# Kernel tuning notes

Measured on AMD Instinct MI355X. Metric: run time of the kernel, lower is better.

## Reference

```python
import jax, jax.numpy as jnp
import numpy as np

MASK_VALUE = -1e6


def setup_inputs() -> dict:
    key = jax.random.key(0)
    ks = jax.random.split(key, 8)
    B, Lq, Lk, D, H = 4, 512, 512, 128, 128
    return {
        "queries": jax.random.normal(ks[0], (B, Lq, D), dtype=jnp.float32),
        "keys": jax.random.normal(ks[1], (B, Lk, D), dtype=jnp.float32),
        "values": jax.random.normal(ks[2], (B, Lk, D), dtype=jnp.float32),
        "valid_seq_len": jax.random.randint(ks[3], (B,), 1, Lk + 1),
        "Wq": jax.random.normal(ks[4], (D, H), dtype=jnp.float32) * 0.05,
        "Wk": jax.random.normal(ks[5], (D, H), dtype=jnp.float32) * 0.05,
        "wv": jax.random.normal(ks[6], (H,), dtype=jnp.float32) * 0.05,
        "Wo": jax.random.normal(ks[7], (D, H), dtype=jnp.float32) * 0.05,
    }


def reference(queries, keys, values, valid_seq_len, Wq, Wk, wv, Wo):
    # q: (B,Lq,H), k: (B,Lk,H)
    q = jnp.einsum("bqd,dh->bqh", queries, Wq)
    k = jnp.einsum("bkd,dh->bkh", keys, Wk)
    # additive features: (B,Lq,Lk,H) -> scalar scores via wv
    feat = jnp.tanh(q[:, :, None, :] + k[:, None, :, :])
    scores = jnp.einsum("bqkh,h->bqk", feat, wv)
    # mask invalid key positions per batch (softmax over last dim)
    Lk = keys.shape[1]
    mask = jnp.arange(Lk)[None, None, :] < valid_seq_len[:, None, None]
    scores = jnp.where(mask, scores, MASK_VALUE)
    attn = jax.nn.softmax(scores, axis=-1)  # (B,Lq,Lk)
    out = jnp.einsum("bqk,bkd->bqd", attn, values)
    return jnp.einsum("bqd,dh->bqh", out, Wo)
```

## Files before the change

### kernel.cpp

```cpp
#include <hip/hip_runtime.h>
#include <hip/hip_bf16.h>

#define B_  4
#define LQ  512
#define LK  512
#define D_  128
#define H_  128
#define TQ  4

#define TWO_LOG2E 2.885390081777927f
#define LOG2E     1.442695040888963f

__device__ __forceinline__ float fexp2(float x) {
#if __has_builtin(__builtin_amdgcn_exp2f)
  return __builtin_amdgcn_exp2f(x);
#else
  return exp2f(x);
#endif
}
__device__ __forceinline__ float frcp(float x) {
#if __has_builtin(__builtin_amdgcn_rcpf)
  return __builtin_amdgcn_rcpf(x);
#else
  return __fdividef(1.0f, x);
#endif
}

__global__ __launch_bounds__(256) void proj_kernel(
    const float* __restrict__ queries, const float* __restrict__ keys,
    const float* __restrict__ Wq, const float* __restrict__ Wk,
    float* __restrict__ qproj, float* __restrict__ kT) {
  __shared__ float s_x[8][D_];
  int r0 = blockIdx.x * 8;
  bool qside = r0 < B_ * LQ;
  const float* X = qside ? queries : keys;
  const float* W = qside ? Wq : Wk;
  int rb = qside ? r0 : r0 - B_ * LQ;
  int tid = threadIdx.x;
  for (int i = tid; i < 8 * D_; i += 256)
    s_x[i >> 7][i & 127] = X[(size_t)(rb + (i >> 7)) * D_ + (i & 127)];
  __syncthreads();
  int h = tid & 127, rh = tid >> 7;
  float a0 = 0.f, a1 = 0.f, a2 = 0.f, a3 = 0.f;
  #pragma unroll 8
  for (int d = 0; d < D_; ++d) {
    float w = W[d * H_ + h];
    a0 += s_x[rh * 4 + 0][d] * w;
    a1 += s_x[rh * 4 + 1][d] * w;
    a2 += s_x[rh * 4 + 2][d] * w;
    a3 += s_x[rh * 4 + 3][d] * w;
  }
  if (qside) {
    qproj[(size_t)(rb + rh * 4 + 0) * H_ + h] = a0 * TWO_LOG2E;
    qproj[(size_t)(rb + rh * 4 + 1) * H_ + h] = a1 * TWO_LOG2E;
    qproj[(size_t)(rb + rh * 4 + 2) * H_ + h] = a2 * TWO_LOG2E;
    qproj[(size_t)(rb + rh * 4 + 3) * H_ + h] = a3 * TWO_LOG2E;
  } else {
    int b = rb >> 9, kk = (rb & 511) + rh * 4;
    float* dst = kT + ((size_t)b * H_ + h) * LK + kk;
    dst[0] = a0 * TWO_LOG2E;
    dst[1] = a1 * TWO_LOG2E;
    dst[2] = a2 * TWO_LOG2E;
    dst[3] = a3 * TWO_LOG2E;
  }
}

__global__ __launch_bounds__(512, 4) void attn_kernel(
    const float* __restrict__ qproj, const float* __restrict__ kT,
    const float* __restrict__ values, const int* __restrict__ vlen_arr,
    const float* __restrict__ wv, const float* __restrict__ Wo,
    float* __restrict__ out) {
  int b  = blockIdx.y;
  int q0 = blockIdx.x * TQ;
  int tid = threadIdx.x;

  __shared__ float s_q[TQ][H_];
  __shared__ float s_wv[H_];
  __shared__ float s_sc[TQ][LK];
  __shared__ float s_po[2][TQ][D_];

  for (int i = tid; i < TQ * H_; i += 512)
    s_q[i >> 7][i & 127] = qproj[(size_t)(b * LQ + q0 + (i >> 7)) * H_ + (i & 127)];
  if (tid < H_) s_wv[tid] = wv[tid];
  __syncthreads();
  int vlen = vlen_arr[b];

  const float4* wv4p = (const float4*)s_wv;
  float sum_wv = 0.f;
  #pragma unroll
  for (int j = 0; j < H_ / 4; ++j) {
    float4 t = wv4p[j];
    sum_wv += t.x + t.y + t.z + t.w;
  }

  {
    int kt = tid & 255, qs = tid >> 8;
    int k  = kt * 2;
    if (k < vlen) {
      const float2* kTp = (const float2*)(kT + (size_t)b * H_ * LK);
      const float4* qap = (const float4*)s_q[qs * 2 + 0];
      const float4* qbp = (const float4*)s_q[qs * 2 + 1];
      float a00 = 0.f, a10 = 0.f, a01 = 0.f, a11 = 0.f;
      #pragma unroll 4
      for (int h4 = 0; h4 < H_ / 4; ++h4) {
        float2 kv0 = kTp[(size_t)(4 * h4 + 0) * 256 + kt];
        float2 kv1 = kTp[(size_t)(4 * h4 + 1) * 256 + kt];
        float2 kv2 = kTp[(size_t)(4 * h4 + 2) * 256 + kt];
        float2 kv3 = kTp[(size_t)(4 * h4 + 3) * 256 + kt];
        float4 w4 = wv4p[h4];
        float4 qa = qap[h4];
        float4 qb = qbp[h4];
        a00 = fmaf(w4.x, frcp(fexp2(qa.x + kv0.x) + 1.f), a00);
        a10 = fmaf(w4.x, frcp(fexp2(qa.x + kv0.y) + 1.f), a10);
        a01 = fmaf(w4.x, frcp(fexp2(qb.x + kv0.x) + 1.f), a01);
        a11 = fmaf(w4.x, frcp(fexp2(qb.x + kv0.y) + 1.f), a11);
        a00 = fmaf(w4.y, frcp(fexp2(qa.y + kv1.x) + 1.f), a00);
        a10 = fmaf(w4.y, frcp(fexp2(qa.y + kv1.y) + 1.f), a10);
        a01 = fmaf(w4.y, frcp(fexp2(qb.y + kv1.x) + 1.f), a01);
        a11 = fmaf(w4.y, frcp(fexp2(qb.y + kv1.y) + 1.f), a11);
        a00 = fmaf(w4.z, frcp(fexp2(qa.z + kv2.x) + 1.f), a00);
        a10 = fmaf(w4.z, frcp(fexp2(qa.z + kv2.y) + 1.f), a10);
        a01 = fmaf(w4.z, frcp(fexp2(qb.z + kv2.x) + 1.f), a01);
        a11 = fmaf(w4.z, frcp(fexp2(qb.z + kv2.y) + 1.f), a11);
        a00 = fmaf(w4.w, frcp(fexp2(qa.w + kv3.x) + 1.f), a00);
        a10 = fmaf(w4.w, frcp(fexp2(qa.w + kv3.y) + 1.f), a10);
        a01 = fmaf(w4.w, frcp(fexp2(qb.w + kv3.x) + 1.f), a01);
        a11 = fmaf(w4.w, frcp(fexp2(qb.w + kv3.y) + 1.f), a11);
      }
      bool m1 = (k + 1) < vlen;
      float2 r0 = { fmaf(-2.f, a00, sum_wv), m1 ? fmaf(-2.f, a10, sum_wv) : -1.0e6f };
      float2 r1 = { fmaf(-2.f, a01, sum_wv), m1 ? fmaf(-2.f, a11, sum_wv) : -1.0e6f };
      ((float2*)s_sc[qs * 2 + 0])[kt] = r0;
      ((float2*)s_sc[qs * 2 + 1])[kt] = r1;
    } else {
      float2 mm = { -1.0e6f, -1.0e6f };
      ((float2*)s_sc[qs * 2 + 0])[kt] = mm;
      ((float2*)s_sc[qs * 2 + 1])[kt] = mm;
    }
  }
  __syncthreads();

  int wave = tid >> 6, lane = tid & 63;

  if (wave < TQ) {
    float m = -3.0e38f;
    #pragma unroll
    for (int j = 0; j < LK / 64; ++j) m = fmaxf(m, s_sc[wave][lane + j * 64]);
    #pragma unroll
    for (int off = 32; off; off >>= 1) m = fmaxf(m, __shfl_xor(m, off));
    float sum = 0.f;
    float vals[LK / 64];
    #pragma unroll
    for (int j = 0; j < LK / 64; ++j) {
      float e = fexp2((s_sc[wave][lane + j * 64] - m) * LOG2E);
      vals[j] = e;
      sum += e;
    }
    #pragma unroll
    for (int off = 32; off; off >>= 1) sum += __shfl_xor(sum, off);
    float inv = frcp(sum);
    #pragma unroll
    for (int j = 0; j < LK / 64; ++j) s_sc[wave][lane + j * 64] = vals[j] * inv;
  }
  __syncthreads();

  {
    int row = wave >> 1, kc = wave & 1;
    int kend = min((((vlen + 3) >> 2) << 2), (kc + 1) * 256);
    const float2* vrow = (const float2*)(values + (size_t)b * LK * D_);
    float2 a = {0.f, 0.f};
    for (int k = kc * 256; k < kend; k += 4) {
      float4 sc4 = *((const float4*)&s_sc[row][k]);
      float2 v0 = vrow[(size_t)(k + 0) * 64 + lane];
      float2 v1 = vrow[(size_t)(k + 1) * 64 + lane];
      float2 v2 = vrow[(size_t)(k + 2) * 64 + lane];
      float2 v3 = vrow[(size_t)(k + 3) * 64 + lane];
      a.x += sc4.x * v0.x + sc4.y * v1.x + sc4.z * v2.x + sc4.w * v3.x;
      a.y += sc4.x * v0.y + sc4.y * v1.y + sc4.z * v2.y + sc4.w * v3.y;
    }
    s_po[kc][row][2 * lane]     = a.x;
    s_po[kc][row][2 * lane + 1] = a.y;
  }
  __syncthreads();

  {
    int ql = tid >> 7, h = tid & 127;
    float acc = 0.f;
    #pragma unroll 8
    for (int d = 0; d < D_; ++d)
      acc += (s_po[0][ql][d] + s_po[1][ql][d]) * Wo[d * H_ + h];
    out[((size_t)b * LQ + q0 + ql) * H_ + h] = acc;
  }
}

extern "C" void kernel_launch(void* const* d_in, const int* in_sizes, int n_in,
                              void* d_out, int out_size, void* d_ws, size_t ws_size,
                              hipStream_t stream) {
  const float* queries = (const float*)d_in[0];
  const float* keys    = (const float*)d_in[1];
  const float* values  = (const float*)d_in[2];
  const int*   vlen    = (const int*)d_in[3];
  const float* Wq      = (const float*)d_in[4];
  const float* Wk      = (const float*)d_in[5];
  const float* wv      = (const float*)d_in[6];
  const float* Wo      = (const float*)d_in[7];
  float* out = (float*)d_out;

  float* qproj = (float*)d_ws;
  float* kT    = qproj + (size_t)B_ * LQ * H_;

  proj_kernel<<<dim3(B_ * (LQ + LK) / 8), 256, 0, stream>>>(queries, keys, Wq, Wk, qproj, kT);
  attn_kernel<<<dim3(LQ / TQ, B_), 512, 0, stream>>>(qproj, kT, values, vlen, wv, Wo, out);
}
```

Measured before the change: 130.9 us.

## Stage key projection tiles in double-buffered LDS and compute 4 queries per thread

The score phase now streams the transposed key projection through a double-buffered shared-memory tile of 16 hidden dims by all keys. The next tile's global load overlaps with the tanh/score computation on the current tile. Each thread now owns one key and all four queries, where before it handled two keys and two queries. The occupancy hint in launch_bounds is dropped, and shared memory grows by 64 KB per block, which may limit how many blocks fit per CU. A barrier per tile is added, and the global load stays unconditional even when a block's valid length is short.

```diff
diff --git a/kernel.cpp b/kernel.cpp
--- a/kernel.cpp
+++ b/kernel.cpp
@@ -7,6 +7,8 @@
 #define D_  128
 #define H_  128
 #define TQ  4
+#define HT  16
+#define NT  (H_ / HT)
 
 #define TWO_LOG2E 2.885390081777927f
 #define LOG2E     1.442695040888963f
@@ -65,7 +67,7 @@
   }
 }
 
-__global__ __launch_bounds__(512, 4) void attn_kernel(
+__global__ __launch_bounds__(512) void attn_kernel(
     const float* __restrict__ qproj, const float* __restrict__ kT,
     const float* __restrict__ values, const int* __restrict__ vlen_arr,
     const float* __restrict__ wv, const float* __restrict__ Wo,
@@ -74,6 +76,7 @@
   int q0 = blockIdx.x * TQ;
   int tid = threadIdx.x;
 
+  __shared__ float s_kt[2][HT][LK];
   __shared__ float s_q[TQ][H_];
   __shared__ float s_wv[H_];
   __shared__ float s_sc[TQ][LK];
@@ -82,6 +85,16 @@
   for (int i = tid; i < TQ * H_; i += 512)
     s_q[i >> 7][i & 127] = qproj[(size_t)(b * LQ + q0 + (i >> 7)) * H_ + (i & 127)];
   if (tid < H_) s_wv[tid] = wv[tid];
+
+  const float4* kt4 = (const float4*)(kT + (size_t)b * H_ * LK);
+
+  {
+    float4 r[4];
+    #pragma unroll
+    for (int j = 0; j < 4; ++j) r[j] = kt4[j * 512 + tid];
+    #pragma unroll
+    for (int j = 0; j < 4; ++j) ((float4*)s_kt[0])[j * 512 + tid] = r[j];
+  }
   __syncthreads();
   int vlen = vlen_arr[b];
 
@@ -89,54 +102,64 @@
   float sum_wv = 0.f;
   #pragma unroll
   for (int j = 0; j < H_ / 4; ++j) {
-    float4 t = wv4p[j];
-    sum_wv += t.x + t.y + t.z + t.w;
-  }
-
-  {
-    int kt = tid & 255, qs = tid >> 8;
-    int k  = kt * 2;
+    float4 t4 = wv4p[j];
+    sum_wv += t4.x + t4.y + t4.z + t4.w;
+  }
+
+  int k = tid;
+  float acc[TQ] = {0.f, 0.f, 0.f, 0.f};
+  for (int t = 0; t < NT; ++t) {
+    int cur = t & 1;
+    float4 r[4];
+    if (t + 1 < NT) {
+      const float4* src = kt4 + (size_t)(t + 1) * (HT * LK / 4);
+      #pragma unroll
+      for (int j = 0; j < 4; ++j) r[j] = src[j * 512 + tid];
+    }
     if (k < vlen) {
-      const float2* kTp = (const float2*)(kT + (size_t)b * H_ * LK);
-      const float4* qap = (const float4*)s_q[qs * 2 + 0];
-      const float4* qbp = (const float4*)s_q[qs * 2 + 1];
-      float a00 = 0.f, a10 = 0.f, a01 = 0.f, a11 = 0.f;
-      #pragma unroll 4
-      for (int h4 = 0; h4 < H_ / 4; ++h4) {
-        float2 kv0 = kTp[(size_t)(4 * h4 + 0) * 256 + kt];
-        float2 kv1 = kTp[(size_t)(4 * h4 + 1) * 256 + kt];
-        float2 kv2 = kTp[(size_t)(4 * h4 + 2) * 256 + kt];
-        float2 kv3 = kTp[(size_t)(4 * h4 + 3) * 256 + kt];
-        float4 w4 = wv4p[h4];
-        float4 qa = qap[h4];
-        float4 qb = qbp[h4];
-        a00 = fmaf(w4.x, frcp(fexp2(qa.x + kv0.x) + 1.f), a00);
-        a10 = fmaf(w4.x, frcp(fexp2(qa.x + kv0.y) + 1.f), a10);
-        a01 = fmaf(w4.x, frcp(fexp2(qb.x + kv0.x) + 1.f), a01);
-        a11 = fmaf(w4.x, frcp(fexp2(qb.x + kv0.y) + 1.f), a11);
-        a00 = fmaf(w4.y, frcp(fexp2(qa.y + kv1.x) + 1.f), a00);
-        a10 = fmaf(w4.y, frcp(fexp2(qa.y + kv1.y) + 1.f), a10);
-        a01 = fmaf(w4.y, frcp(fexp2(qb.y + kv1.x) + 1.f), a01);
-        a11 = fmaf(w4.y, frcp(fexp2(qb.y + kv1.y) + 1.f), a11);
-        a00 = fmaf(w4.z, frcp(fexp2(qa.z + kv2.x) + 1.f), a00);
-        a10 = fmaf(w4.z, frcp(fexp2(qa.z + kv2.y) + 1.f), a10);
-        a01 = fmaf(w4.z, frcp(fexp2(qb.z + kv2.x) + 1.f), a01);
-        a11 = fmaf(w4.z, frcp(fexp2(qb.z + kv2.y) + 1.f), a11);
-        a00 = fmaf(w4.w, frcp(fexp2(qa.w + kv3.x) + 1.f), a00);
-        a10 = fmaf(w4.w, frcp(fexp2(qa.w + kv3.y) + 1.f), a10);
-        a01 = fmaf(w4.w, frcp(fexp2(qb.w + kv3.x) + 1.f), a01);
-        a11 = fmaf(w4.w, frcp(fexp2(qb.w + kv3.y) + 1.f), a11);
+      #pragma unroll
+      for (int hh4 = 0; hh4 < HT / 4; ++hh4) {
+        int hb = t * HT + hh4 * 4;
+        float4 w4  = *(const float4*)&s_wv[hb];
+        float4 qv0 = *(const float4*)&s_q[0][hb];
+        float4 qv1 = *(const float4*)&s_q[1][hb];
+        float4 qv2 = *(const float4*)&s_q[2][hb];
+        float4 qv3 = *(const float4*)&s_q[3][hb];
+        float kv0 = s_kt[cur][hh4 * 4 + 0][k];
+        float kv1 = s_kt[cur][hh4 * 4 + 1][k];
+        float kv2 = s_kt[cur][hh4 * 4 + 2][k];
+        float kv3 = s_kt[cur][hh4 * 4 + 3][k];
+        acc[0] = fmaf(w4.x, frcp(fexp2(qv0.x + kv0) + 1.f), acc[0]);
+        acc[1] = fmaf(w4.x, frcp(fexp2(qv1.x + kv0) + 1.f), acc[1]);
+        acc[2] = fmaf(w4.x, frcp(fexp2(qv2.x + kv0) + 1.f), acc[2]);
+        acc[3] = fmaf(w4.x, frcp(fexp2(qv3.x + kv0) + 1.f), acc[3]);
+        acc[0] = fmaf(w4.y, frcp(fexp2(qv0.y + kv1) + 1.f), acc[0]);
+        acc[1] = fmaf(w4.y, frcp(fexp2(qv1.y + kv1) + 1.f), acc[1]);
+        acc[2] = fmaf(w4.y, frcp(fexp2(qv2.y + kv1) + 1.f), acc[2]);
+        acc[3] = fmaf(w4.y, frcp(fexp2(qv3.y + kv1) + 1.f), acc[3]);
+        acc[0] = fmaf(w4.z, frcp(fexp2(qv0.z + kv2) + 1.f), acc[0]);
+        acc[1] = fmaf(w4.z, frcp(fexp2(qv1.z + kv2) + 1.f), acc[1]);
+        acc[2] = fmaf(w4.z, frcp(fexp2(qv2.z + kv2) + 1.f), acc[2]);
+        acc[3] = fmaf(w4.z, frcp(fexp2(qv3.z + kv2) + 1.f), acc[3]);
+        acc[0] = fmaf(w4.w, frcp(fexp2(qv0.w + kv3) + 1.f), acc[0]);
+        acc[1] = fmaf(w4.w, frcp(fexp2(qv1.w + kv3) + 1.f), acc[1]);
+        acc[2] = fmaf(w4.w, frcp(fexp2(qv2.w + kv3) + 1.f), acc[2]);
+        acc[3] = fmaf(w4.w, frcp(fexp2(qv3.w + kv3) + 1.f), acc[3]);
       }
-      bool m1 = (k + 1) < vlen;
-      float2 r0 = { fmaf(-2.f, a00, sum_wv), m1 ? fmaf(-2.f, a10, sum_wv) : -1.0e6f };
-      float2 r1 = { fmaf(-2.f, a01, sum_wv), m1 ? fmaf(-2.f, a11, sum_wv) : -1.0e6f };
-      ((float2*)s_sc[qs * 2 + 0])[kt] = r0;
-      ((float2*)s_sc[qs * 2 + 1])[kt] = r1;
-    } else {
-      float2 mm = { -1.0e6f, -1.0e6f };
-      ((float2*)s_sc[qs * 2 + 0])[kt] = mm;
-      ((float2*)s_sc[qs * 2 + 1])[kt] = mm;
-    }
+    }
+    if (t + 1 < NT) {
+      float4* dst = (float4*)s_kt[cur ^ 1];
+      #pragma unroll
+      for (int j = 0; j < 4; ++j) dst[j * 512 + tid] = r[j];
+    }
+    __syncthreads();
+  }
+  if (k < vlen) {
+    #pragma unroll
+    for (int q = 0; q < TQ; ++q) s_sc[q][k] = fmaf(-2.f, acc[q], sum_wv);
+  } else {
+    #pragma unroll
+    for (int q = 0; q < TQ; ++q) s_sc[q][k] = -1.0e6f;
   }
   __syncthreads();
 
@@ -169,12 +192,12 @@
     int kend = min((((vlen + 3) >> 2) << 2), (kc + 1) * 256);
     const float2* vrow = (const float2*)(values + (size_t)b * LK * D_);
     float2 a = {0.f, 0.f};
-    for (int k = kc * 256; k < kend; k += 4) {
-      float4 sc4 = *((const float4*)&s_sc[row][k]);
-      float2 v0 = vrow[(size_t)(k + 0) * 64 + lane];
-      float2 v1 = vrow[(size_t)(k + 1) * 64 + lane];
-      float2 v2 = vrow[(size_t)(k + 2) * 64 + lane];
-      float2 v3 = vrow[(size_t)(k + 3) * 64 + lane];
+    for (int kk = kc * 256; kk < kend; kk += 4) {
+      float4 sc4 = *((const float4*)&s_sc[row][kk]);
+      float2 v0 = vrow[(size_t)(kk + 0) * 64 + lane];
+      float2 v1 = vrow[(size_t)(kk + 1) * 64 + lane];
+      float2 v2 = vrow[(size_t)(kk + 2) * 64 + lane];
+      float2 v3 = vrow[(size_t)(kk + 3) * 64 + lane];
       a.x += sc4.x * v0.x + sc4.y * v1.x + sc4.z * v2.x + sc4.w * v3.x;
       a.y += sc4.x * v0.y + sc4.y * v1.y + sc4.z * v2.y + sc4.w * v3.y;
     }
@@ -185,11 +208,11 @@
 
   {
     int ql = tid >> 7, h = tid & 127;
-    float acc = 0.f;
+    float acc2 = 0.f;
     #pragma unroll 8
     for (int d = 0; d < D_; ++d)
-      acc += (s_po[0][ql][d] + s_po[1][ql][d]) * Wo[d * H_ + h];
-    out[((size_t)b * LQ + q0 + ql) * H_ + h] = acc;
+      acc2 += (s_po[0][ql][d] + s_po[1][ql][d]) * Wo[d * H_ + h];
+    out[((size_t)b * LQ + q0 + ql) * H_ + h] = acc2;
   }
 }
 
```

After: 135.4 us. 3.4% more time.

## Halve query tile per block and remap threads to one key each

Applied to the files above, without the earlier changes.

The query tile per attention block drops from 4 rows to 2, which doubles the grid. The score phase now gives each thread one key for both queries instead of two keys. The PV product is split into four key chunks reduced in shared memory, and the minimum-blocks launch bound is removed. The aim is more blocks and waves in flight to hide the exp/rcp and global-load latency, at the cost of half the reuse of kT and value loads, so global/L2 traffic roughly doubles.

```diff
diff --git a/kernel.cpp b/kernel.cpp
--- a/kernel.cpp
+++ b/kernel.cpp
@@ -6,7 +6,7 @@
 #define LK  512
 #define D_  128
 #define H_  128
-#define TQ  4
+#define TQ  2
 
 #define TWO_LOG2E 2.885390081777927f
 #define LOG2E     1.442695040888963f
@@ -65,7 +65,7 @@
   }
 }
 
-__global__ __launch_bounds__(512, 4) void attn_kernel(
+__global__ __launch_bounds__(512) void attn_kernel(
     const float* __restrict__ qproj, const float* __restrict__ kT,
     const float* __restrict__ values, const int* __restrict__ vlen_arr,
     const float* __restrict__ wv, const float* __restrict__ Wo,
@@ -77,11 +77,12 @@
   __shared__ float s_q[TQ][H_];
   __shared__ float s_wv[H_];
   __shared__ float s_sc[TQ][LK];
-  __shared__ float s_po[2][TQ][D_];
-
-  for (int i = tid; i < TQ * H_; i += 512)
-    s_q[i >> 7][i & 127] = qproj[(size_t)(b * LQ + q0 + (i >> 7)) * H_ + (i & 127)];
-  if (tid < H_) s_wv[tid] = wv[tid];
+  __shared__ float s_po[4][TQ][D_];
+
+  if (tid < TQ * H_)
+    s_q[tid >> 7][tid & 127] = qproj[(size_t)(b * LQ + q0 + (tid >> 7)) * H_ + (tid & 127)];
+  else if (tid < TQ * H_ + H_)
+    s_wv[tid - TQ * H_] = wv[tid - TQ * H_];
   __syncthreads();
   int vlen = vlen_arr[b];
 
@@ -89,54 +90,39 @@
   float sum_wv = 0.f;
   #pragma unroll
   for (int j = 0; j < H_ / 4; ++j) {
-    float4 t = wv4p[j];
-    sum_wv += t.x + t.y + t.z + t.w;
-  }
-
-  {
-    int kt = tid & 255, qs = tid >> 8;
-    int k  = kt * 2;
-    if (k < vlen) {
-      const float2* kTp = (const float2*)(kT + (size_t)b * H_ * LK);
-      const float4* qap = (const float4*)s_q[qs * 2 + 0];
-      const float4* qbp = (const float4*)s_q[qs * 2 + 1];
-      float a00 = 0.f, a10 = 0.f, a01 = 0.f, a11 = 0.f;
-      #pragma unroll 4
-      for (int h4 = 0; h4 < H_ / 4; ++h4) {
-        float2 kv0 = kTp[(size_t)(4 * h4 + 0) * 256 + kt];
-        float2 kv1 = kTp[(size_t)(4 * h4 + 1) * 256 + kt];
-        float2 kv2 = kTp[(size_t)(4 * h4 + 2) * 256 + kt];
-        float2 kv3 = kTp[(size_t)(4 * h4 + 3) * 256 + kt];
-        float4 w4 = wv4p[h4];
-        float4 qa = qap[h4];
-        float4 qb = qbp[h4];
-        a00 = fmaf(w4.x, frcp(fexp2(qa.x + kv0.x) + 1.f), a00);
-        a10 = fmaf(w4.x, frcp(fexp2(qa.x + kv0.y) + 1.f), a10);
-        a01 = fmaf(w4.x, frcp(fexp2(qb.x + kv0.x) + 1.f), a01);
-        a11 = fmaf(w4.x, frcp(fexp2(qb.x + kv0.y) + 1.f), a11);
-        a00 = fmaf(w4.y, frcp(fexp2(qa.y + kv1.x) + 1.f), a00);
-        a10 = fmaf(w4.y, frcp(fexp2(qa.y + kv1.y) + 1.f), a10);
-        a01 = fmaf(w4.y, frcp(fexp2(qb.y + kv1.x) + 1.f), a01);
-        a11 = fmaf(w4.y, frcp(fexp2(qb.y + kv1.y) + 1.f), a11);
-        a00 = fmaf(w4.z, frcp(fexp2(qa.z + kv2.x) + 1.f), a00);
-        a10 = fmaf(w4.z, frcp(fexp2(qa.z + kv2.y) + 1.f), a10);
-        a01 = fmaf(w4.z, frcp(fexp2(qb.z + kv2.x) + 1.f), a01);
-        a11 = fmaf(w4.z, frcp(fexp2(qb.z + kv2.y) + 1.f), a11);
-        a00 = fmaf(w4.w, frcp(fexp2(qa.w + kv3.x) + 1.f), a00);
-        a10 = fmaf(w4.w, frcp(fexp2(qa.w + kv3.y) + 1.f), a10);
-        a01 = fmaf(w4.w, frcp(fexp2(qb.w + kv3.x) + 1.f), a01);
-        a11 = fmaf(w4.w, frcp(fexp2(qb.w + kv3.y) + 1.f), a11);
-      }
-      bool m1 = (k + 1) < vlen;
-      float2 r0 = { fmaf(-2.f, a00, sum_wv), m1 ? fmaf(-2.f, a10, sum_wv) : -1.0e6f };
-      float2 r1 = { fmaf(-2.f, a01, sum_wv), m1 ? fmaf(-2.f, a11, sum_wv) : -1.0e6f };
-      ((float2*)s_sc[qs * 2 + 0])[kt] = r0;
-      ((float2*)s_sc[qs * 2 + 1])[kt] = r1;
-    } else {
-      float2 mm = { -1.0e6f, -1.0e6f };
-      ((float2*)s_sc[qs * 2 + 0])[kt] = mm;
-      ((float2*)s_sc[qs * 2 + 1])[kt] = mm;
-    }
+    float4 t4 = wv4p[j];
+    sum_wv += t4.x + t4.y + t4.z + t4.w;
+  }
+
+  int k = tid;
+  if (k < vlen) {
+    const float* kcol = kT + ((size_t)b * H_) * LK + k;
+    const float4* qap = (const float4*)s_q[0];
+    const float4* qbp = (const float4*)s_q[1];
+    float acc0 = 0.f, acc1 = 0.f;
+    #pragma unroll 4
+    for (int h4 = 0; h4 < H_ / 4; ++h4) {
+      float kv0 = kcol[(size_t)(4 * h4 + 0) * LK];
+      float kv1 = kcol[(size_t)(4 * h4 + 1) * LK];
+      float kv2 = kcol[(size_t)(4 * h4 + 2) * LK];
+      float kv3 = kcol[(size_t)(4 * h4 + 3) * LK];
+      float4 w4 = wv4p[h4];
+      float4 qa = qap[h4];
+      float4 qb = qbp[h4];
+      acc0 = fmaf(w4.x, frcp(fexp2(qa.x + kv0) + 1.f), acc0);
+      acc1 = fmaf(w4.x, frcp(fexp2(qb.x + kv0) + 1.f), acc1);
+      acc0 = fmaf(w4.y, frcp(fexp2(qa.y + kv1) + 1.f), acc0);
+      acc1 = fmaf(w4.y, frcp(fexp2(qb.y + kv1) + 1.f), acc1);
+      acc0 = fmaf(w4.z, frcp(fexp2(qa.z + kv2) + 1.f), acc0);
+      acc1 = fmaf(w4.z, frcp(fexp2(qb.z + kv2) + 1.f), acc1);
+      acc0 = fmaf(w4.w, frcp(fexp2(qa.w + kv3) + 1.f), acc0);
+      acc1 = fmaf(w4.w, frcp(fexp2(qb.w + kv3) + 1.f), acc1);
+    }
+    s_sc[0][k] = fmaf(-2.f, acc0, sum_wv);
+    s_sc[1][k] = fmaf(-2.f, acc1, sum_wv);
+  } else {
+    s_sc[0][k] = -1.0e6f;
+    s_sc[1][k] = -1.0e6f;
   }
   __syncthreads();
 
@@ -165,16 +151,16 @@
   __syncthreads();
 
   {
-    int row = wave >> 1, kc = wave & 1;
-    int kend = min((((vlen + 3) >> 2) << 2), (kc + 1) * 256);
+    int row = wave >> 2, kc = wave & 3;
+    int kend = min((((vlen + 3) >> 2) << 2), (kc + 1) * 128);
     const float2* vrow = (const float2*)(values + (size_t)b * LK * D_);
     float2 a = {0.f, 0.f};
-    for (int k = kc * 256; k < kend; k += 4) {
-      float4 sc4 = *((const float4*)&s_sc[row][k]);
-      float2 v0 = vrow[(size_t)(k + 0) * 64 + lane];
-      float2 v1 = vrow[(size_t)(k + 1) * 64 + lane];
-      float2 v2 = vrow[(size_t)(k + 2) * 64 + lane];
-      float2 v3 = vrow[(size_t)(k + 3) * 64 + lane];
+    for (int kk = kc * 128; kk < kend; kk += 4) {
+      float4 sc4 = *((const float4*)&s_sc[row][kk]);
+      float2 v0 = vrow[(size_t)(kk + 0) * 64 + lane];
+      float2 v1 = vrow[(size_t)(kk + 1) * 64 + lane];
+      float2 v2 = vrow[(size_t)(kk + 2) * 64 + lane];
+      float2 v3 = vrow[(size_t)(kk + 3) * 64 + lane];
       a.x += sc4.x * v0.x + sc4.y * v1.x + sc4.z * v2.x + sc4.w * v3.x;
       a.y += sc4.x * v0.y + sc4.y * v1.y + sc4.z * v2.y + sc4.w * v3.y;
     }
@@ -183,13 +169,15 @@
   }
   __syncthreads();
 
-  {
+  if (tid < TQ * H_) {
     int ql = tid >> 7, h = tid & 127;
-    float acc = 0.f;
+    float acc2 = 0.f;
     #pragma unroll 8
-    for (int d = 0; d < D_; ++d)
-      acc += (s_po[0][ql][d] + s_po[1][ql][d]) * Wo[d * H_ + h];
-    out[((size_t)b * LQ + q0 + ql) * H_ + h] = acc;
+    for (int d = 0; d < D_; ++d) {
+      float po = s_po[0][ql][d] + s_po[1][ql][d] + s_po[2][ql][d] + s_po[3][ql][d];
+      acc2 = fmaf(po, Wo[d * H_ + h], acc2);
+    }
+    out[((size_t)b * LQ + q0 + ql) * H_ + h] = acc2;
   }
 }
 
```

New measurement: 154.8 us. 18.2% more time.
